# Optimization experiments

Measured on AMD Instinct MI355X. Metric: run time of the kernel, lower is better.

The kernel has to match this reference:

```python
import jax, jax.numpy as jnp
import numpy as np

K, D, N = 32, 128, 65536
EPS = 1e-6


def setup_inputs() -> dict:
    key = jax.random.key(0)
    k1, k2, k3 = jax.random.split(key, 3)
    x = jax.random.normal(k1, (N, D), dtype=jnp.float32)
    means = jax.random.normal(k2, (K, D), dtype=jnp.float32)
    # SPD covariances (original init is identity; use SPD perturbation so Cholesky is valid)
    B = jax.random.normal(k3, (K, D, D), dtype=jnp.float32) * 0.1
    covariances = jnp.einsum('kij,klj->kil', B, B) / D + jnp.eye(D, dtype=jnp.float32)
    weights = jnp.ones((K,), dtype=jnp.float32) / K
    return {"x": x, "means": means, "covariances": covariances, "weights": weights}


def reference(x, means, covariances, weights):
    d = x.shape[-1]
    cov = covariances + EPS * jnp.eye(d, dtype=x.dtype)          # [K,D,D]
    L = jnp.linalg.cholesky(cov)                                 # [K,D,D]
    diff = x[None, :, :] - means[:, None, :]                     # [K,N,D]
    # Mahalanobis via triangular solve: m = ||L^{-1}(x-mu)||^2
    sol = jax.scipy.linalg.solve_triangular(
        L, jnp.swapaxes(diff, 1, 2), lower=True)                 # [K,D,N]
    maha = jnp.sum(sol * sol, axis=1)                            # [K,N]
    half_logdet = jnp.sum(jnp.log(jnp.diagonal(L, axis1=1, axis2=2)), axis=1)  # [K]
    log_prob = (-0.5 * (d * jnp.log(2.0 * jnp.pi) + maha)
                - half_logdet[:, None])                          # [K,N]
    weighted = log_prob.T + jnp.log(weights)                     # [N,K]
    return jax.nn.logsumexp(weighted, axis=1)                    # [N]
```

## Files before the change

kernel.cpp:

```cpp
#include <hip/hip_runtime.h>
#include <hip/hip_bf16.h>
#include <math.h>

#define KCOMP 32
#define DDIM  128
#define NPTS  65536
#define GMM_EPS 1e-6f
#define SA 129
#define UFT 1280

typedef __attribute__((ext_vector_type(8)))  __bf16 bf16x8;
typedef __attribute__((ext_vector_type(16))) float  f32x16;

__device__ __forceinline__ unsigned short f2bf(float f){
  unsigned u = __builtin_bit_cast(unsigned, f);
  u = (u + 0x7FFFu + ((u >> 16) & 1u)) >> 16;
  return (unsigned short)u;
}
__device__ __forceinline__ float rlane(float v, int lsrc){
  return __builtin_bit_cast(float, __builtin_amdgcn_readlane(__builtin_bit_cast(int, v), lsrc));
}

__device__ __noinline__ float chol_inv32(float* __restrict__ Ab,
                                         float* __restrict__ Wb,
                                         const int c){
  float ar[32], lr[32], rd[32], v[32];
  #pragma unroll
  for(int i=0;i<32;i++) ar[i] = Ab[i*SA + c];
  float hl = 0.f;
  #pragma unroll
  for(int j=0;j<32;j++){
    float d   = rlane(ar[j], j);
    float rsd = rsqrtf(d);
    hl += logf(d);
    rd[j] = rsd;
    float Lcj  = ar[j]*rsd;
    lr[j] = (c>=j) ? Lcj : 0.f;
    float coef = Lcj*rsd;
    #pragma unroll
    for(int i=j;i<32;i++){
      float bij = rlane(ar[i], j);
      ar[i] = fmaf(-bij, coef, ar[i]);
    }
  }
  #pragma unroll
  for(int j=0;j<32;j++) Ab[c*SA + j] = lr[j];
  #pragma unroll
  for(int i=0;i<32;i++){
    float s = (i==c) ? 1.f : 0.f;
    #pragma unroll
    for(int p=0;p<i;p++) s = fmaf(-rlane(lr[p], i), v[p], s);
    v[i] = s * rd[i];
  }
  #pragma unroll
  for(int i=0;i<32;i++) Wb[i*SA + c] = v[i];
  return 0.5f*hl;
}

__global__ __launch_bounds__(256) void k_prep(const float* __restrict__ cov,
                                              const float* __restrict__ wts,
                                              const float* __restrict__ means,
                                              float* __restrict__ ws_c3,
                                              unsigned short* __restrict__ qfrag,
                                              unsigned short* __restrict__ ufrag){
  __shared__ float A[DDIM*SA];
  __shared__ float W[DDIM*SA];
  __shared__ float Tb[3*32*33];
  __shared__ float muS[DDIM];
  const int t=threadIdx.x, w=t>>6, l=t&63, k=blockIdx.x;
  const int r0=(l>>3)*4, c0=(l&7)*4;

  const float4* cv4 = (const float4*)(cov + (size_t)k*DDIM*DDIM);
  #pragma unroll
  for(int v=0; v<16; v++){
    int idx4 = t + 256*v; float4 f = cv4[idx4];
    int e = idx4*4; int i = e>>7; int j = e&127;
    float* d = &A[i*SA+j]; d[0]=f.x; d[1]=f.y; d[2]=f.z; d[3]=f.w;
  }
  for(int z=t; z<DDIM*SA; z+=256) W[z] = 0.f;
  if(t<DDIM) muS[t] = means[k*DDIM+t];
  __syncthreads();
  if(t<DDIM) A[t*SA+t] += GMM_EPS;
  __syncthreads();

  static const int SYI[10]={1,2,2,3,3,3, 2,3,3, 3};
  static const int SYJ[10]={1,1,2,1,2,3, 2,2,3, 3};
  static const int SYO[5] ={0,6,9,10,10};

  float hsum = 0.f;
  #pragma unroll 1
  for(int b=0;b<4;b++){
    const int b32=b*32;
    if(w==0) hsum += chol_inv32(&A[b32*SA+b32], &W[b32*SA+b32], l&31);
    __syncthreads();
    if(w < 3-b){
      const int ibl = b+1+w;
      float acc[4][4]={};
      for(int kc=0;kc<32;kc+=4){
        float a_[4][4], b_[4][4];
        #pragma unroll
        for(int e=0;e<4;e++)
          #pragma unroll
          for(int g=0;g<4;g++){
            a_[e][g]=A[(32*ibl+r0+e)*SA + b32+kc+g];
            b_[e][g]=W[(b32+c0+e)*SA   + b32+kc+g];
          }
        #pragma unroll
        for(int e=0;e<4;e++)
          #pragma unroll
          for(int f=0;f<4;f++)
            acc[e][f]+=a_[e][0]*b_[f][0]+a_[e][1]*b_[f][1]
                      +a_[e][2]*b_[f][2]+a_[e][3]*b_[f][3];
      }
      #pragma unroll
      for(int e=0;e<4;e++)
        #pragma unroll
        for(int f=0;f<4;f++)
          A[(32*ibl+r0+e)*SA + b32+c0+f] = acc[e][f];
    }
    __syncthreads();
    #pragma unroll 1
    for(int u=SYO[b]+w; u<SYO[b+1]; u+=4){
      const int ui=SYI[u], uj=SYJ[u];
      float acc[4][4]={};
      for(int kc=0;kc<32;kc+=4){
        float a_[4][4], b_[4][4];
        #pragma unroll
        for(int e=0;e<4;e++)
          #pragma unroll
          for(int g=0;g<4;g++){
            a_[e][g]=A[(32*ui+r0+e)*SA + b32+kc+g];
            b_[e][g]=A[(32*uj+c0+e)*SA + b32+kc+g];
          }
        #pragma unroll
        for(int e=0;e<4;e++)
          #pragma unroll
          for(int f=0;f<4;f++)
            acc[e][f]+=a_[e][0]*b_[f][0]+a_[e][1]*b_[f][1]
                      +a_[e][2]*b_[f][2]+a_[e][3]*b_[f][3];
      }
      #pragma unroll
      for(int e=0;e<4;e++)
        #pragma unroll
        for(int f=0;f<4;f++)
          A[(32*ui+r0+e)*SA+32*uj+c0+f] -= acc[e][f];
    }
    __syncthreads();
  }

  #pragma unroll 1
  for(int lev=1;lev<=3;lev++){
    if(w<4-lev){
      const int j=w, i=w+lev;
      float* T=&Tb[w*1056];
      float acc[4][4]={};
      #pragma unroll 1
      for(int p=j;p<i;p++){
        for(int kc=0;kc<32;kc+=4){
          float a_[4][4], b_[4][4];
          #pragma unroll
          for(int e=0;e<4;e++)
            #pragma unroll
            for(int g=0;g<4;g++){
              a_[e][g]=A[(32*i+r0+e)*SA + 32*p+kc+g];
              b_[e][g]=W[(32*p+kc+e)*SA + 32*j+c0+g];
            }
          #pragma unroll
          for(int e=0;e<4;e++)
            #pragma unroll
            for(int f=0;f<4;f++)
              acc[e][f]+=a_[e][0]*b_[0][f]+a_[e][1]*b_[1][f]
                        +a_[e][2]*b_[2][f]+a_[e][3]*b_[3][f];
        }
      }
      #pragma unroll
      for(int e=0;e<4;e++)
        #pragma unroll
        for(int f=0;f<4;f++)
          T[(r0+e)*33+c0+f]=acc[e][f];
      float ac2[4][4]={};
      for(int kc=0;kc<32;kc+=4){
        float a_[4][4], b_[4][4];
        #pragma unroll
        for(int e=0;e<4;e++)
          #pragma unroll
          for(int g=0;g<4;g++){
            a_[e][g]=W[(32*i+r0+e)*SA + 32*i+kc+g];
            b_[e][g]=T[(kc+e)*33 + c0+g];
          }
        #pragma unroll
        for(int e=0;e<4;e++)
          #pragma unroll
          for(int f=0;f<4;f++)
            ac2[e][f]+=a_[e][0]*b_[0][f]+a_[e][1]*b_[1][f]
                      +a_[e][2]*b_[2][f]+a_[e][3]*b_[3][f];
      }
      #pragma unroll
      for(int e=0;e<4;e++)
        #pragma unroll
        for(int f=0;f<4;f++)
          W[(32*i+r0+e)*SA+32*j+c0+f] = -ac2[e][f];
    }
    __syncthreads();
  }

  if(t<DDIM){
    float s=0.f;
    #pragma unroll 8
    for(int c=0;c<DDIM;c++) s += W[t*SA+c]*muS[c];
    Tb[t]=s;
  }
  __syncthreads();
  if(t<DDIM){
    float s=0.f;
    #pragma unroll 8
    for(int r=0;r<DDIM;r++) s += W[r*SA+t]*Tb[r];
    Tb[128+t]=s;
  }
  __syncthreads();
  if(w==0){
    float p = Tb[l]*Tb[l] + Tb[l+64]*Tb[l+64];
    #pragma unroll
    for(int off=32; off; off>>=1) p += __shfl_xor(p, off);
    if(l==0) ws_c3[k] = logf(wts[k]) - hsum - 117.6241322f - 0.5f*p;
  }
  if(t<16){
    int tile=t>>1, half=t&1;
    const float* qq=&Tb[128 + tile*16 + half*8];
    unsigned uu[4];
    #pragma unroll
    for(int h2=0;h2<4;h2++){
      unsigned lo=f2bf(qq[2*h2]), hi=f2bf(qq[2*h2+1]);
      uu[h2]=lo|(hi<<16);
    }
    uint4 wv; wv.x=uu[0]; wv.y=uu[1]; wv.z=uu[2]; wv.w=uu[3];
    ((uint4*)qfrag)[tile*64 + half*32 + k] = wv;
  }
  #pragma unroll 1
  for(int s0=t;s0<UFT;s0+=256){
    int tile=s0>>6, l2=s0&63;
    int db = (tile<2)?0:((tile<6)?1:((tile<12)?2:3));
    int kc = tile - ((db==0)?0:((db==1)?2:((db==2)?6:12)));
    int row=db*32+(l2&31), colb=kc*16+((l2>>5)<<3);
    unsigned uu[4];
    #pragma unroll
    for(int h2=0;h2<4;h2++){
      unsigned lo=f2bf(W[row*SA+colb+2*h2]);
      unsigned hi=f2bf(W[row*SA+colb+2*h2+1]);
      uu[h2]=lo|(hi<<16);
    }
    uint4 wv; wv.x=uu[0]; wv.y=uu[1]; wv.z=uu[2]; wv.w=uu[3];
    ((uint4*)ufrag)[(size_t)k*UFT+s0]=wv;
  }
}

#define TM0(j) ((j)<2 ? (j) : (j)+10)
#define TM1(j) ((j)+2)

#define RUNLOOP(EXTA_, TM) {                                                  \
    const uint4* ufb = uf;                                                    \
    _Pragma("unroll")                                                         \
    for(int j=0;j<5;j++) uA[j]=ufb[(size_t)(TM(j))*64+lane];                  \
    _Pragma("unroll 1")                                                       \
    for(int k2=0;k2<KCOMP;k2++){                                              \
      _Pragma("unroll")                                                       \
      for(int j=0;j<5;j++) uB[j]=ufb[(size_t)(TM(j+5))*64+lane];              \
      const uint4* ufn = uf + (size_t)((k2+1)&(KCOMP-1))*UFT;                 \
      f32x16 aA={}, aB={};                                                    \
      _Pragma("unroll")                                                       \
      for(int j=0;j<5;j++){                                                   \
        bf16x8 fr=__builtin_bit_cast(bf16x8,uA[j]);                           \
        if(j<(EXTA_)) aA=__builtin_amdgcn_mfma_f32_32x32x16_bf16(fr,xf[j],aA,0,0,0); \
        else          aB=__builtin_amdgcn_mfma_f32_32x32x16_bf16(fr,xf[j-(EXTA_)],aB,0,0,0); \
      }                                                                       \
      _Pragma("unroll")                                                       \
      for(int j=0;j<5;j++) uA[j]=ufn[(size_t)(TM(j))*64+lane];                \
      _Pragma("unroll")                                                       \
      for(int j=5;j<10;j++){                                                  \
        bf16x8 fr=__builtin_bit_cast(bf16x8,uB[j-5]);                         \
        aB=__builtin_amdgcn_mfma_f32_32x32x16_bf16(fr,xf[j-(EXTA_)],aB,0,0,0);\
      }                                                                       \
      float p0=0.f,p1=0.f,p2=0.f,p3=0.f;                                      \
      _Pragma("unroll")                                                       \
      for(int r=0;r<16;r+=2){                                                 \
        p0=fmaf(aA[r],aA[r],p0);   p1=fmaf(aA[r+1],aA[r+1],p1);               \
        p2=fmaf(aB[r],aB[r],p2);   p3=fmaf(aB[r+1],aB[r+1],p3);               \
      }                                                                       \
      atomicAdd(&maha[k2*64 + ptb + ln], (p0+p1)+(p2+p3));                    \
      ufb = ufn;                                                              \
    }                                                                         \
  }

__global__ __launch_bounds__(256,4) void k_main(const float* __restrict__ x,
                                                const uint4* __restrict__ uf,
                                                const uint4* __restrict__ qf,
                                                const float* __restrict__ ws_c3,
                                                float* __restrict__ out){
  __shared__ float maha[KCOMP*64];
  __shared__ float c3s[KCOMP];
  const int t = threadIdx.x, lane = t&63, w = t>>6;
  const int qh = lane>>5, ln = lane&31;
  const int pt = w>>1, sel = w&1, ptb = pt*32;
  const size_t n0 = (size_t)blockIdx.x * 64;

  uint4 qr[8];
  if(sel==0){
    #pragma unroll
    for(int c=0;c<8;c++) qr[c]=qf[c*64+lane];
  }
  if(t < KCOMP) c3s[t] = ws_c3[t];

  bf16x8 xf[8];
  {
    const float* rowp = x + (n0 + (size_t)(ptb + ln))*DDIM + 8*qh;
    #pragma unroll
    for(int c=0; c<8; c++){
      float4 f0 = *(const float4*)(rowp + c*16);
      float4 f1 = *(const float4*)(rowp + c*16 + 4);
      union { unsigned short us[8]; bf16x8 v; } cvt;
      cvt.us[0]=f2bf(f0.x); cvt.us[1]=f2bf(f0.y); cvt.us[2]=f2bf(f0.z); cvt.us[3]=f2bf(f0.w);
      cvt.us[4]=f2bf(f1.x); cvt.us[5]=f2bf(f1.y); cvt.us[6]=f2bf(f1.z); cvt.us[7]=f2bf(f1.w);
      xf[c] = cvt.v;
    }
  }

  if(sel==0){
    f32x16 aq = {};
    #pragma unroll
    for(int c=0;c<8;c++)
      aq = __builtin_amdgcn_mfma_f32_32x32x16_bf16(
             __builtin_bit_cast(bf16x8, qr[c]), xf[c], aq, 0,0,0);
    #pragma unroll
    for(int r=0;r<16;r++){
      int row = (r&3) + 8*(r>>2) + 4*qh;
      maha[row*64 + ptb + ln] = -2.f*aq[r];
    }
  }
  __syncthreads();

  uint4 uA[5], uB[5];
  if(sel==0){ RUNLOOP(2, TM0) } else { RUNLOOP(4, TM1) }
  __syncthreads();

  if(t < 64){
    float m_run = -INFINITY, s_run = 0.f;
    #pragma unroll 1
    for(int k3=0;k3<KCOMP;k3++){
      float a  = c3s[k3] - 0.5f*maha[k3*64 + t];
      float nm = fmaxf(m_run, a);
      s_run = s_run*__expf(m_run-nm) + __expf(a-nm);
      m_run = nm;
    }
    out[n0 + t] = m_run + logf(s_run);
  }
}

extern "C" void kernel_launch(void* const* d_in, const int* in_sizes, int n_in,
                              void* d_out, int out_size, void* d_ws, size_t ws_size,
                              hipStream_t stream){
  const float* x   = (const float*)d_in[0];
  const float* mu  = (const float*)d_in[1];
  const float* cov = (const float*)d_in[2];
  const float* wts = (const float*)d_in[3];
  float* out = (float*)d_out;
  char*  ws  = (char*)d_ws;

  float*          wsC3 = (float*)ws;
  unsigned short* wsQF = (unsigned short*)(ws + 512);
  unsigned short* wsUF = (unsigned short*)(ws + 16384);

  k_prep<<<KCOMP, 256, 0, stream>>>(cov, wts, mu, wsC3, wsQF, wsUF);
  k_main<<<NPTS/64, 256, 0, stream>>>(x, (const uint4*)wsUF, (const uint4*)wsQF, wsC3, out);
}
```

Baseline: 207.9 us.

## Restructure main kernel: stage x in LDS, one component per wave

The main kernel now processes 128 points per 512-thread block. The x tile is converted to bf16 and staged once in shared memory. Each wave holds all 20 triangular-factor fragments of one component in registers and sweeps four 32-point tiles, so factor data is reused instead of being streamed per component from global memory. LDS atomics are replaced by per-wave writes, and the logsumexp is done online in four chunks of eight components. The trade-offs are higher register pressure from 20 uint4 fragments per lane, extra block-wide barriers, and half as many blocks.

```diff
diff --git a/kernel.cpp b/kernel.cpp
--- a/kernel.cpp
+++ b/kernel.cpp
@@ -254,105 +254,104 @@
   }
 }
 
-#define TM0(j) ((j)<2 ? (j) : (j)+10)
-#define TM1(j) ((j)+2)
-
-#define RUNLOOP(EXTA_, TM) {                                                  \
-    const uint4* ufb = uf;                                                    \
-    _Pragma("unroll")                                                         \
-    for(int j=0;j<5;j++) uA[j]=ufb[(size_t)(TM(j))*64+lane];                  \
-    _Pragma("unroll 1")                                                       \
-    for(int k2=0;k2<KCOMP;k2++){                                              \
-      _Pragma("unroll")                                                       \
-      for(int j=0;j<5;j++) uB[j]=ufb[(size_t)(TM(j+5))*64+lane];              \
-      const uint4* ufn = uf + (size_t)((k2+1)&(KCOMP-1))*UFT;                 \
-      f32x16 aA={}, aB={};                                                    \
-      _Pragma("unroll")                                                       \
-      for(int j=0;j<5;j++){                                                   \
-        bf16x8 fr=__builtin_bit_cast(bf16x8,uA[j]);                           \
-        if(j<(EXTA_)) aA=__builtin_amdgcn_mfma_f32_32x32x16_bf16(fr,xf[j],aA,0,0,0); \
-        else          aB=__builtin_amdgcn_mfma_f32_32x32x16_bf16(fr,xf[j-(EXTA_)],aB,0,0,0); \
-      }                                                                       \
-      _Pragma("unroll")                                                       \
-      for(int j=0;j<5;j++) uA[j]=ufn[(size_t)(TM(j))*64+lane];                \
-      _Pragma("unroll")                                                       \
-      for(int j=5;j<10;j++){                                                  \
-        bf16x8 fr=__builtin_bit_cast(bf16x8,uB[j-5]);                         \
-        aB=__builtin_amdgcn_mfma_f32_32x32x16_bf16(fr,xf[j-(EXTA_)],aB,0,0,0);\
-      }                                                                       \
-      float p0=0.f,p1=0.f,p2=0.f,p3=0.f;                                      \
-      _Pragma("unroll")                                                       \
-      for(int r=0;r<16;r+=2){                                                 \
-        p0=fmaf(aA[r],aA[r],p0);   p1=fmaf(aA[r+1],aA[r+1],p1);               \
-        p2=fmaf(aB[r],aB[r],p2);   p3=fmaf(aB[r+1],aB[r+1],p3);               \
-      }                                                                       \
-      atomicAdd(&maha[k2*64 + ptb + ln], (p0+p1)+(p2+p3));                    \
-      ufb = ufn;                                                              \
-    }                                                                         \
-  }
-
-__global__ __launch_bounds__(256,4) void k_main(const float* __restrict__ x,
+#define MFMA_B(acc,u,xv) acc=__builtin_amdgcn_mfma_f32_32x32x16_bf16(__builtin_bit_cast(bf16x8,u),xv,acc,0,0,0)
+
+__global__ __launch_bounds__(512,2) void k_main(const float* __restrict__ x,
                                                 const uint4* __restrict__ uf,
                                                 const uint4* __restrict__ qf,
                                                 const float* __restrict__ ws_c3,
                                                 float* __restrict__ out){
-  __shared__ float maha[KCOMP*64];
+  __shared__ uint4 xs[4*8*64];
+  __shared__ float lin[KCOMP*128];
+  __shared__ float mahaS[8*128];
   __shared__ float c3s[KCOMP];
-  const int t = threadIdx.x, lane = t&63, w = t>>6;
-  const int qh = lane>>5, ln = lane&31;
-  const int pt = w>>1, sel = w&1, ptb = pt*32;
-  const size_t n0 = (size_t)blockIdx.x * 64;
-
-  uint4 qr[8];
-  if(sel==0){
-    #pragma unroll
-    for(int c=0;c<8;c++) qr[c]=qf[c*64+lane];
-  }
-  if(t < KCOMP) c3s[t] = ws_c3[t];
-
-  bf16x8 xf[8];
+  const int t=threadIdx.x, lane=t&63, w=t>>6;
+  const int qh=lane>>5, ln=lane&31;
+  const size_t n0=(size_t)blockIdx.x*128;
+
+  if(t<KCOMP) c3s[t]=ws_c3[t];
+
   {
-    const float* rowp = x + (n0 + (size_t)(ptb + ln))*DDIM + 8*qh;
-    #pragma unroll
-    for(int c=0; c<8; c++){
-      float4 f0 = *(const float4*)(rowp + c*16);
-      float4 f1 = *(const float4*)(rowp + c*16 + 4);
-      union { unsigned short us[8]; bf16x8 v; } cvt;
-      cvt.us[0]=f2bf(f0.x); cvt.us[1]=f2bf(f0.y); cvt.us[2]=f2bf(f0.z); cvt.us[3]=f2bf(f0.w);
-      cvt.us[4]=f2bf(f1.x); cvt.us[5]=f2bf(f1.y); cvt.us[6]=f2bf(f1.z); cvt.us[7]=f2bf(f1.w);
-      xf[c] = cvt.v;
-    }
-  }
-
-  if(sel==0){
-    f32x16 aq = {};
-    #pragma unroll
-    for(int c=0;c<8;c++)
-      aq = __builtin_amdgcn_mfma_f32_32x32x16_bf16(
-             __builtin_bit_cast(bf16x8, qr[c]), xf[c], aq, 0,0,0);
+    const float* xb = x + n0*DDIM;
+    #pragma unroll
+    for(int j=0;j<8;j++){
+      int idx = j*512 + t;
+      int n = idx & 127, d0 = (idx>>7)*4;
+      float4 f = *(const float4*)(xb + (size_t)n*DDIM + d0);
+      unsigned lo = f2bf(f.x) | (((unsigned)f2bf(f.y))<<16);
+      unsigned hi = f2bf(f.z) | (((unsigned)f2bf(f.w))<<16);
+      int tile=n>>5, lnn=n&31, c=d0>>4, qq=(d0>>3)&1, e4=d0&7;
+      *(uint2*)((char*)xs + tile*8192 + c*1024 + qq*512 + lnn*16 + e4*2)
+          = make_uint2(lo,hi);
+    }
+  }
+  __syncthreads();
+
+  if(w<4){
+    f32x16 aq={};
+    #pragma unroll
+    for(int c=0;c<8;c++){
+      uint4 qr = qf[c*64+lane];
+      bf16x8 xq = __builtin_bit_cast(bf16x8, xs[w*512 + c*64 + lane]);
+      MFMA_B(aq, qr, xq);
+    }
     #pragma unroll
     for(int r=0;r<16;r++){
-      int row = (r&3) + 8*(r>>2) + 4*qh;
-      maha[row*64 + ptb + ln] = -2.f*aq[r];
-    }
-  }
-  __syncthreads();
-
-  uint4 uA[5], uB[5];
-  if(sel==0){ RUNLOOP(2, TM0) } else { RUNLOOP(4, TM1) }
-  __syncthreads();
-
-  if(t < 64){
-    float m_run = -INFINITY, s_run = 0.f;
+      int row=(r&3)+8*(r>>2)+4*qh;
+      lin[row*128 + w*32 + ln] = -2.f*aq[r];
+    }
+  }
+  __syncthreads();
+
+  float m_run=-INFINITY, s_run=0.f;
+
+  #pragma unroll 1
+  for(int iter=0;iter<4;iter++){
+    const int k = iter*8 + w;
+    uint4 ur[20];
+    #pragma unroll
+    for(int j=0;j<20;j++) ur[j]=uf[(size_t)k*UFT + j*64 + lane];
+
     #pragma unroll 1
-    for(int k3=0;k3<KCOMP;k3++){
-      float a  = c3s[k3] - 0.5f*maha[k3*64 + t];
-      float nm = fmaxf(m_run, a);
-      s_run = s_run*__expf(m_run-nm) + __expf(a-nm);
-      m_run = nm;
-    }
-    out[n0 + t] = m_run + logf(s_run);
-  }
+    for(int tile=0;tile<4;tile++){
+      bf16x8 xf[8];
+      #pragma unroll
+      for(int c=0;c<8;c++) xf[c]=__builtin_bit_cast(bf16x8, xs[tile*512 + c*64 + lane]);
+      f32x16 a0={},a1={},a2={},a3={};
+      #pragma unroll
+      for(int c=0;c<2;c++) MFMA_B(a0, ur[c],    xf[c]);
+      #pragma unroll
+      for(int c=0;c<4;c++) MFMA_B(a1, ur[2+c],  xf[c]);
+      #pragma unroll
+      for(int c=0;c<6;c++) MFMA_B(a2, ur[6+c],  xf[c]);
+      #pragma unroll
+      for(int c=0;c<8;c++) MFMA_B(a3, ur[12+c], xf[c]);
+      float p0=0.f,p1=0.f,p2=0.f,p3=0.f;
+      #pragma unroll
+      for(int r=0;r<16;r+=2){
+        p0=fmaf(a0[r],a0[r],p0); p1=fmaf(a0[r+1],a0[r+1],p1);
+        p2=fmaf(a1[r],a1[r],p2); p3=fmaf(a1[r+1],a1[r+1],p3);
+        p0=fmaf(a2[r],a2[r],p0); p1=fmaf(a2[r+1],a2[r+1],p1);
+        p2=fmaf(a3[r],a3[r],p2); p3=fmaf(a3[r+1],a3[r+1],p3);
+      }
+      float p=(p0+p1)+(p2+p3);
+      p += __shfl_xor(p,32);
+      if(qh==0) mahaS[w*128 + tile*32 + ln] = p;
+    }
+    __syncthreads();
+    if(t<128){
+      #pragma unroll
+      for(int c8=0;c8<8;c8++){
+        int k2=iter*8+c8;
+        float a  = c3s[k2] - 0.5f*(mahaS[c8*128+t] + lin[k2*128+t]);
+        float nm = fmaxf(m_run,a);
+        s_run = s_run*__expf(m_run-nm)+__expf(a-nm);
+        m_run = nm;
+      }
+    }
+    __syncthreads();
+  }
+  if(t<128) out[n0+t] = m_run + logf(s_run);
 }
 
 extern "C" void kernel_launch(void* const* d_in, const int* in_sizes, int n_in,
@@ -370,5 +369,5 @@
   unsigned short* wsUF = (unsigned short*)(ws + 16384);
 
   k_prep<<<KCOMP, 256, 0, stream>>>(cov, wts, mu, wsC3, wsQF, wsUF);
-  k_main<<<NPTS/64, 256, 0, stream>>>(x, (const uint4*)wsUF, (const uint4*)wsQF, wsC3, out);
-}
+  k_main<<<NPTS/128, 512, 0, stream>>>(x, (const uint4*)wsUF, (const uint4*)wsQF, wsC3, out);
+}
```

Measured after the change: 196.3 us. 1.06x faster.
